# Optimization experiments

Measured on AMD Instinct MI355X. Metric: run time of the kernel, lower is better.

## Reference

```python
import jax, jax.numpy as jnp
import numpy as np

IN_FEATURES = 4096
OUT_FEATURES = 32000


def setup_inputs() -> dict:
    key = jax.random.key(0)
    kx, kw, ks, kb = jax.random.split(key, 4)
    x = jax.random.normal(kx, (16, 1, IN_FEATURES), dtype=jnp.float32)
    # int8 weight buffer, per torch.randint(-128, 127, ...)
    weight_int8 = jax.random.randint(kw, (OUT_FEATURES, IN_FEATURES), -128, 127, dtype=jnp.int8)
    scale = jax.random.uniform(ks, (OUT_FEATURES, 1), dtype=jnp.float32)
    bias = jax.random.uniform(kb, (1, OUT_FEATURES), dtype=jnp.float32)
    return {"x": x, "weight_int8": weight_int8, "scale": scale, "bias": bias}


def reference(x, weight_int8, scale, bias):
    # F.linear(x, W.type_as(x)): upcast int8 weight to activation dtype, then matmul
    w = weight_int8.astype(x.dtype)               # [O, I]
    out = jnp.einsum('bsi,oi->bso', x, w)         # [B, S, O]
    out = out * scale.T                           # per-output-channel scale, [1, O] broadcast
    out = out + bias                              # [1, O] broadcast
    return out.astype(x.dtype)
```

## Files before the change

### kernel.cpp

```cpp
#include <hip/hip_runtime.h>

#define IN_F  4096
#define OUT_F 32000
#define KC    128
#define NT    (IN_F / KC)

typedef __attribute__((ext_vector_type(8))) short bf16x8;
typedef __attribute__((ext_vector_type(4))) float f32x4;

__device__ __forceinline__ short bf(float f) {
    __bf16 h = (__bf16)f;
    short s;
    __builtin_memcpy(&s, &h, 2);
    return s;
}

__global__ __launch_bounds__(256) void w8a16_kernel(
    const int* __restrict__ W, const float* __restrict__ X,
    const float* __restrict__ scale, const float* __restrict__ bias,
    float* __restrict__ out)
{
    __shared__ __align__(16) short Wl[2][64][KC];
    __shared__ __align__(16) short Xl[2][16][KC];

    const int tid  = threadIdx.x;
    const int lane = tid & 63;
    const int wave = tid >> 6;
    const int n    = lane & 15;
    const int kg   = lane >> 4;
    const int lo   = lane & 31;
    const int hi   = lane >> 5;
    const int o_base = blockIdx.x * 64;

    int4   wreg[8];
    float4 xreg[2];
    f32x4  acc = {0.f, 0.f, 0.f, 0.f};

    #define LOAD_TILE(t)                                                          \
        _Pragma("unroll")                                                         \
        for (int j = 0; j < 8; ++j) {                                             \
            const int r = wave * 16 + 2 * j + hi;                                 \
            wreg[j] = *reinterpret_cast<const int4*>(                             \
                W + (size_t)(o_base + r) * IN_F + (t) * KC + lo * 4);             \
        }                                                                         \
        _Pragma("unroll")                                                         \
        for (int j = 0; j < 2; ++j) {                                             \
            const int r = wave * 4 + 2 * j + hi;                                  \
            xreg[j] = *reinterpret_cast<const float4*>(                           \
                X + (size_t)r * IN_F + (t) * KC + lo * 4);                        \
        }

    #define CVT_WRITE(buf)                                                        \
        _Pragma("unroll")                                                         \
        for (int j = 0; j < 8; ++j) {                                             \
            const int r = wave * 16 + 2 * j + hi;                                 \
            short4 v;                                                             \
            v.x = bf((float)wreg[j].x); v.y = bf((float)wreg[j].y);               \
            v.z = bf((float)wreg[j].z); v.w = bf((float)wreg[j].w);               \
            char* p = (char*)&Wl[buf][r][0] + ((lo * 8) ^ ((r & 7) << 4));        \
            *reinterpret_cast<short4*>(p) = v;                                    \
        }                                                                         \
        _Pragma("unroll")                                                         \
        for (int j = 0; j < 2; ++j) {                                             \
            const int r = wave * 4 + 2 * j + hi;                                  \
            short4 v;                                                             \
            v.x = bf(xreg[j].x); v.y = bf(xreg[j].y);                             \
            v.z = bf(xreg[j].z); v.w = bf(xreg[j].w);                             \
            char* p = (char*)&Xl[buf][r][0] + ((lo * 8) ^ ((r & 7) << 4));        \
            *reinterpret_cast<short4*>(p) = v;                                    \
        }

    const int rA  = wave * 16 + n;
    const int swzA = (n & 7) << 4;

    #define COMPUTE(buf)                                                          \
        _Pragma("unroll")                                                         \
        for (int s = 0; s < KC / 32; ++s) {                                       \
            const int off = (s * 64 + kg * 16) ^ swzA;                            \
            bf16x8 a = *reinterpret_cast<const bf16x8*>(                          \
                (const char*)&Wl[buf][rA][0] + off);                              \
            bf16x8 b = *reinterpret_cast<const bf16x8*>(                          \
                (const char*)&Xl[buf][n][0] + off);                               \
            acc = __builtin_amdgcn_mfma_f32_16x16x32_bf16(a, b, acc, 0, 0, 0);    \
        }

    LOAD_TILE(0);
    CVT_WRITE(0);
    __syncthreads();

    for (int t = 0; t < NT; ++t) {
        const int cur = t & 1;
        if (t + 1 < NT) { LOAD_TILE(t + 1); }
        COMPUTE(cur);
        if (t + 1 < NT) { CVT_WRITE(cur ^ 1); }
        __syncthreads();
    }

    const int o = o_base + wave * 16 + kg * 4;
    const float4 sc = *reinterpret_cast<const float4*>(scale + o);
    const float4 bs = *reinterpret_cast<const float4*>(bias + o);
    float4 rr;
    rr.x = acc[0] * sc.x + bs.x;
    rr.y = acc[1] * sc.y + bs.y;
    rr.z = acc[2] * sc.z + bs.z;
    rr.w = acc[3] * sc.w + bs.w;
    *reinterpret_cast<float4*>(out + (size_t)n * OUT_F + o) = rr;

    #undef LOAD_TILE
    #undef CVT_WRITE
    #undef COMPUTE
}

extern "C" void kernel_launch(void* const* d_in, const int* in_sizes, int n_in,
                              void* d_out, int out_size, void* d_ws, size_t ws_size,
                              hipStream_t stream) {
    const float* x     = (const float*)d_in[0];
    const int*   w     = (const int*)  d_in[1];
    const float* scale = (const float*)d_in[2];
    const float* bias  = (const float*)d_in[3];
    float* out = (float*)d_out;
    (void)in_sizes; (void)n_in; (void)d_ws; (void)ws_size; (void)out_size;

    w8a16_kernel<<<dim3(OUT_F / 64), dim3(256), 0, stream>>>(w, x, scale, bias, out);
}
```

Measured before the change: 101.5 us.

## Stream int32 weight tiles directly to LDS with global_load_lds and convert at compute

Weight tiles are now copied from global memory straight into shared memory using the direct global-to-LDS load path with a swizzle applied on the global address side, instead of going through registers. The int-to-bf16 conversion moves from the write stage into the compute loop, where each lane reads its int32 values from LDS and converts them before the MFMA. This removes the register staging for weights and may improve latency hiding, but it doubles LDS usage for weights (64 KB for W) and duplicates conversion work at read time. The kernel is bound by the 4-byte-per-weight global read, so any gain depends on better overlap.

```diff
diff --git a/kernel.cpp b/kernel.cpp
--- a/kernel.cpp
+++ b/kernel.cpp
@@ -7,6 +7,7 @@
 
 typedef __attribute__((ext_vector_type(8))) short bf16x8;
 typedef __attribute__((ext_vector_type(4))) float f32x4;
+typedef unsigned int u32;
 
 __device__ __forceinline__ short bf(float f) {
     __bf16 h = (__bf16)f;
@@ -15,12 +16,22 @@
     return s;
 }
 
+__device__ __forceinline__ void gload16(const void* g, void* l) {
+    __builtin_amdgcn_global_load_lds(
+        (const __attribute__((address_space(1))) u32*)g,
+        (__attribute__((address_space(3))) u32*)l, 16, 0, 0);
+}
+
+__device__ __forceinline__ int swzW(int r) {
+    return ((r & 7) << 5) | (((r >> 3) & 1) << 4);
+}
+
 __global__ __launch_bounds__(256) void w8a16_kernel(
     const int* __restrict__ W, const float* __restrict__ X,
     const float* __restrict__ scale, const float* __restrict__ bias,
     float* __restrict__ out)
 {
-    __shared__ __align__(16) short Wl[2][64][KC];
+    __shared__ __align__(16) int   Wl[2][64][KC];
     __shared__ __align__(16) short Xl[2][16][KC];
 
     const int tid  = threadIdx.x;
@@ -32,17 +43,10 @@
     const int hi   = lane >> 5;
     const int o_base = blockIdx.x * 64;
 
-    int4   wreg[8];
     float4 xreg[2];
     f32x4  acc = {0.f, 0.f, 0.f, 0.f};
 
-    #define LOAD_TILE(t)                                                          \
-        _Pragma("unroll")                                                         \
-        for (int j = 0; j < 8; ++j) {                                             \
-            const int r = wave * 16 + 2 * j + hi;                                 \
-            wreg[j] = *reinterpret_cast<const int4*>(                             \
-                W + (size_t)(o_base + r) * IN_F + (t) * KC + lo * 4);             \
-        }                                                                         \
+    #define LOADX(t)                                                              \
         _Pragma("unroll")                                                         \
         for (int j = 0; j < 2; ++j) {                                             \
             const int r = wave * 4 + 2 * j + hi;                                  \
@@ -50,16 +54,17 @@
                 X + (size_t)r * IN_F + (t) * KC + lo * 4);                        \
         }
 
-    #define CVT_WRITE(buf)                                                        \
+    #define GLOADW(buf, t)                                                        \
         _Pragma("unroll")                                                         \
         for (int j = 0; j < 8; ++j) {                                             \
-            const int r = wave * 16 + 2 * j + hi;                                 \
-            short4 v;                                                             \
-            v.x = bf((float)wreg[j].x); v.y = bf((float)wreg[j].y);               \
-            v.z = bf((float)wreg[j].z); v.w = bf((float)wreg[j].w);               \
-            char* p = (char*)&Wl[buf][r][0] + ((lo * 8) ^ ((r & 7) << 4));        \
-            *reinterpret_cast<short4*>(p) = v;                                    \
-        }                                                                         \
+            const int r  = wave * 16 + 2 * j + hi;                                \
+            const char* gp = (const char*)W                                       \
+                + ((size_t)(o_base + r) * IN_F + (size_t)(t) * KC) * 4            \
+                + ((lo * 16) ^ swzW(r));                                          \
+            gload16(gp, &Wl[buf][wave * 16 + 2 * j][0]);                          \
+        }
+
+    #define XWRITE(buf)                                                           \
         _Pragma("unroll")                                                         \
         for (int j = 0; j < 2; ++j) {                                             \
             const int r = wave * 4 + 2 * j + hi;                                  \
@@ -70,29 +75,42 @@
             *reinterpret_cast<short4*>(p) = v;                                    \
         }
 
-    const int rA  = wave * 16 + n;
-    const int swzA = (n & 7) << 4;
+    const int rA    = wave * 16 + n;
+    const int swzA  = swzW(rA);
+    const int swzAx = (n & 7) << 4;
 
     #define COMPUTE(buf)                                                          \
         _Pragma("unroll")                                                         \
         for (int s = 0; s < KC / 32; ++s) {                                       \
-            const int off = (s * 64 + kg * 16) ^ swzA;                            \
-            bf16x8 a = *reinterpret_cast<const bf16x8*>(                          \
-                (const char*)&Wl[buf][rA][0] + off);                              \
+            const int o0 = (s * 128 + kg * 32) ^ swzA;                            \
+            const int4 qa = *reinterpret_cast<const int4*>(                       \
+                (const char*)&Wl[buf][rA][0] + o0);                               \
+            const int4 qb = *reinterpret_cast<const int4*>(                       \
+                (const char*)&Wl[buf][rA][0] + (o0 ^ 16));                        \
+            bf16x8 a;                                                             \
+            a[0]=bf((float)qa.x); a[1]=bf((float)qa.y);                           \
+            a[2]=bf((float)qa.z); a[3]=bf((float)qa.w);                           \
+            a[4]=bf((float)qb.x); a[5]=bf((float)qb.y);                           \
+            a[6]=bf((float)qb.z); a[7]=bf((float)qb.w);                           \
+            const int ox = (s * 64 + kg * 16) ^ swzAx;                            \
             bf16x8 b = *reinterpret_cast<const bf16x8*>(                          \
-                (const char*)&Xl[buf][n][0] + off);                               \
+                (const char*)&Xl[buf][n][0] + ox);                                \
             acc = __builtin_amdgcn_mfma_f32_16x16x32_bf16(a, b, acc, 0, 0, 0);    \
         }
 
-    LOAD_TILE(0);
-    CVT_WRITE(0);
+    LOADX(0);
+    GLOADW(0, 0);
+    XWRITE(0);
     __syncthreads();
 
     for (int t = 0; t < NT; ++t) {
         const int cur = t & 1;
-        if (t + 1 < NT) { LOAD_TILE(t + 1); }
+        if (t + 1 < NT) {
+            LOADX(t + 1);
+            GLOADW(cur ^ 1, t + 1);
+        }
         COMPUTE(cur);
-        if (t + 1 < NT) { CVT_WRITE(cur ^ 1); }
+        if (t + 1 < NT) { XWRITE(cur ^ 1); }
         __syncthreads();
     }
 
@@ -106,8 +124,9 @@
     rr.w = acc[3] * sc.w + bs.w;
     *reinterpret_cast<float4*>(out + (size_t)n * OUT_F + o) = rr;
 
-    #undef LOAD_TILE
-    #undef CVT_WRITE
+    #undef LOADX
+    #undef GLOADW
+    #undef XWRITE
     #undef COMPUTE
 }
 
```

Measured after the change: 98.61 us. 2.8% less time.
